# Performance work log

Measured on AMD Instinct MI355X. Metric: run time of the kernel, lower is better.

## Reference

```python
import jax, jax.numpy as jnp
import numpy as np

B = 256      # graph pairs
N = 256      # nodes per graph (uniform -> padding is a reshape)
DEG = 16     # avg degree
D = 32       # one_hot_dim
F1, F2, F3 = 128, 64, 64
T = 16       # tensor_neurons
BINS = 16
BOT = 16     # bottle_neck_neurons


def setup_inputs() -> dict:
    key = jax.random.key(0)
    ks = jax.random.split(key, 24)
    NT = B * N            # total nodes per side
    NE = B * N * DEG      # total directed edges per side
    x_q = jax.random.normal(ks[0], (NT, D), jnp.float32)
    x_c = jax.random.normal(ks[1], (NT, D), jnp.float32)
    edge_q = jax.random.randint(ks[2], (2, NE), 0, NT, jnp.int32)
    edge_c = jax.random.randint(ks[3], (2, NE), 0, NT, jnp.int32)
    qgraph_sizes = jnp.full((B,), N, jnp.int32)
    cgraph_sizes = jnp.full((B,), N, jnp.int32)

    def glorot(k, shape):
        fan = sum(shape[-2:]) if len(shape) >= 2 else shape[0] * 2
        return jax.random.uniform(k, shape, jnp.float32, -1.0, 1.0) * np.sqrt(6.0 / fan)

    params = dict(
        W1=glorot(ks[4], (D, F1)), b1=jnp.zeros((F1,), jnp.float32),
        W2=glorot(ks[5], (F1, F2)), b2=jnp.zeros((F2,), jnp.float32),
        W3=glorot(ks[6], (F2, F3)), b3=jnp.zeros((F3,), jnp.float32),
        attn_w=glorot(ks[7], (F3, F3)),
        ntn_a_w=glorot(ks[8], (T, F3, F3)),
        ntn_b_w=glorot(ks[9], (2 * F3, T)),
        ntn_bias=glorot(ks[10], (T, 1)),
        fc1_w=glorot(ks[11], (T + BINS, BOT)), fc1_b=jnp.zeros((BOT,), jnp.float32),
        fc2_w=glorot(ks[12], (BOT, 1)), fc2_b=jnp.zeros((1,), jnp.float32),
    )
    return dict(x_q=x_q, edge_q=edge_q, x_c=x_c, edge_c=edge_c,
                qgraph_sizes=qgraph_sizes, cgraph_sizes=cgraph_sizes, **params)


def _gcn(x, src, dst, W, b):
    n = x.shape[0]
    h = x @ W
    loop = jnp.arange(n, dtype=src.dtype)
    s = jnp.concatenate([src, loop])
    d = jnp.concatenate([dst, loop])
    deg = jax.ops.segment_sum(jnp.ones(s.shape, h.dtype), d, num_segments=n)
    dinv = jnp.where(deg > 0, jax.lax.rsqrt(jnp.maximum(deg, 1.0)), 0.0)
    coef = (dinv[s] * dinv[d])[:, None]
    return jax.ops.segment_sum(h[s] * coef, d, num_segments=n) + b


def _gnn(x, ei, W1, b1, W2, b2, W3, b3):
    src, dst = ei[0], ei[1]
    h = jax.nn.relu(_gcn(x, src, dst, W1, b1))        # dropout is identity in eval
    h = jax.nn.relu(_gcn(h, src, dst, W2, b2))
    return _gcn(h, src, dst, W3, b3)                  # [B*N, F3]


def _att_pool(q, attn_w, sizes):
    # q: [B, N, F3]
    ctx = jnp.tanh((q.sum(axis=1) @ attn_w) / sizes.astype(q.dtype)[:, None])  # [B, F3]
    sig = jax.nn.sigmoid(jnp.einsum('bnf,bf->bn', q, ctx))                      # [B, N]
    return jnp.einsum('bnf,bn->bf', q, sig)                                     # [B, F3]


def _pair_hist(q, c):
    # per-pair histogram of q @ c^T with BINS bins over each pair's [min, max]
    s = jax.lax.stop_gradient(jnp.einsum('bnf,bmf->bnm', q, c))  # [B, N, N]
    mn = s.min(axis=(1, 2), keepdims=True)
    mx = s.max(axis=(1, 2), keepdims=True)
    idx = jnp.clip(jnp.floor((s - mn) / jnp.maximum(mx - mn, 1e-12) * BINS),
                   0, BINS - 1).astype(jnp.int32)
    gid = (idx + jnp.arange(B, dtype=jnp.int32)[:, None, None] * BINS).reshape(-1)
    h = jax.ops.segment_sum(jnp.ones(gid.shape, jnp.float32), gid,
                            num_segments=B * BINS).reshape(B, BINS)
    return h / h.sum(axis=1, keepdims=True)


def reference(x_q, edge_q, x_c, edge_c, qgraph_sizes, cgraph_sizes,
              W1, b1, W2, b2, W3, b3, attn_w, ntn_a_w, ntn_b_w, ntn_bias,
              fc1_w, fc1_b, fc2_w, fc2_b):
    q = _gnn(x_q, edge_q, W1, b1, W2, b2, W3, b3).reshape(B, N, F3)
    c = _gnn(x_c, edge_c, W1, b1, W2, b2, W3, b3).reshape(B, N, F3)
    e1 = _att_pool(q, attn_w, qgraph_sizes)
    e2 = _att_pool(c, attn_w, cgraph_sizes)
    ntn = (jnp.einsum('bi,tij,bj->bt', e1, ntn_a_w, e2)
           + jnp.concatenate([e1, e2], axis=-1) @ ntn_b_w
           + ntn_bias[:, 0])
    scores = jax.nn.relu(ntn)                                   # [B, T]
    hist = _pair_hist(q, c)                                     # [B, BINS]
    scores = jnp.concatenate([scores, hist], axis=1)
    scores = jax.nn.relu(scores @ fc1_w + fc1_b)
    p = jax.nn.sigmoid(scores @ fc2_w + fc2_b)[:, 0]            # [B]
    ged = -0.5 * (qgraph_sizes + cgraph_sizes).astype(p.dtype) * jnp.log(p)
    return ged
```

## Files before the change

### kernel.cpp

```cpp
#include <hip/hip_runtime.h>
#include <hip/hip_bf16.h>
#include <math.h>

#define BB 256
#define NN 256
#define NT (BB*NN)
#define NT2 (2*NT)
#define NE (NT*16)
#define DD 32
#define F1C 128
#define F2C 64
#define F3C 64
#define TT 16
#define BINS 16

#define NBUCK 256
#define BSHIFT 9
#define BNODES 512
#define BCAP 10240
#define EPB 4096

typedef __attribute__((ext_vector_type(8))) short short8;
typedef __attribute__((ext_vector_type(4))) float f32x4;
typedef __attribute__((ext_vector_type(2))) float f32x2;

__device__ inline float b2f(ushort u) { return __uint_as_float(((uint)u) << 16); }
__device__ inline ushort f2b(float f) {
    uint u = __float_as_uint(f);
    return (ushort)((u + 0x7fffu + ((u >> 16) & 1u)) >> 16);
}
__device__ inline float clamp8(float v) { return fminf(fmaxf(v, -448.0f), 448.0f); }
__device__ inline uchar f2f8(float v) {
    int r = __builtin_amdgcn_cvt_pk_fp8_f32(clamp8(v), 0.0f, 0, false);
    return (uchar)(r & 0xff);
}
__device__ inline void f8x8_acc(uint2 w, float* acc) {
    f32x2 p;
    p = __builtin_amdgcn_cvt_pk_f32_fp8(w.x, false); acc[0] += p.x; acc[1] += p.y;
    p = __builtin_amdgcn_cvt_pk_f32_fp8(w.x, true);  acc[2] += p.x; acc[3] += p.y;
    p = __builtin_amdgcn_cvt_pk_f32_fp8(w.y, false); acc[4] += p.x; acc[5] += p.y;
    p = __builtin_amdgcn_cvt_pk_f32_fp8(w.y, true);  acc[6] += p.x; acc[7] += p.y;
}
__device__ inline uint2 f8x8_pack(const float* v) {
    uint2 r;
    r.x = (uint)__builtin_amdgcn_cvt_pk_fp8_f32(clamp8(v[0]), clamp8(v[1]), 0, false);
    r.x = (uint)__builtin_amdgcn_cvt_pk_fp8_f32(clamp8(v[2]), clamp8(v[3]), (int)r.x, true);
    r.y = (uint)__builtin_amdgcn_cvt_pk_fp8_f32(clamp8(v[4]), clamp8(v[5]), 0, false);
    r.y = (uint)__builtin_amdgcn_cvt_pk_fp8_f32(clamp8(v[6]), clamp8(v[7]), (int)r.y, true);
    return r;
}

__global__ __launch_bounds__(256) void zero_k(int* __restrict__ gcount) {
    gcount[threadIdx.x] = 0;
}

__global__ __launch_bounds__(256) void p1cvt_k(const int* __restrict__ eq, const int* __restrict__ ec,
                                               uint* __restrict__ staged, int* __restrict__ gcount,
                                               const float* __restrict__ a, const float* __restrict__ b,
                                               ushort* __restrict__ out,
                                               const float* __restrict__ W1, const float* __restrict__ W2,
                                               const float* __restrict__ W3, ushort* __restrict__ Wt1,
                                               ushort* __restrict__ Wt2, uchar* __restrict__ Wt3f8) {
    int t = threadIdx.x;
    if (blockIdx.x < 512) {
        __shared__ uint s_pk[EPB];
        __shared__ int s_cnt[NBUCK];
        __shared__ int s_off[NBUCK];
        __shared__ int s_base[NBUCK];
        __shared__ int s_gb[NBUCK];
        bool sideB = blockIdx.x >= 256;
        const int* edge = sideB ? ec : eq;
        int off = sideB ? NT : 0;
        int e0 = (blockIdx.x & 255) * EPB;
        s_cnt[t] = 0;
        __syncthreads();
        uint pk[16]; int bk[16];
#pragma unroll
        for (int j = 0; j < 16; j++) {
            int e = e0 + j * 256 + t;
            int s = edge[e] + off;
            int d = edge[NE + e] + off;
            bk[j] = d >> BSHIFT;
            pk[j] = ((uint)s << BSHIFT) | (uint)(d & (BNODES - 1));
            atomicAdd(&s_cnt[bk[j]], 1);
        }
        __syncthreads();
        s_off[t] = s_cnt[t];
        __syncthreads();
        for (int o = 1; o < NBUCK; o <<= 1) {
            int x = (t >= o) ? s_off[t - o] : 0;
            __syncthreads();
            s_off[t] += x;
            __syncthreads();
        }
        {
            int ex = s_off[t] - s_cnt[t];
            s_base[t] = ex;
            s_off[t] = ex;
            s_gb[t] = atomicAdd(&gcount[t], s_cnt[t]);
        }
        __syncthreads();
#pragma unroll
        for (int j = 0; j < 16; j++) {
            int pos = atomicAdd(&s_off[bk[j]], 1);
            s_pk[pos] = pk[j];
        }
        __syncthreads();
        int w = t >> 6, l = t & 63;
        int bsel = l >> 4, l16 = l & 15;
        for (int pb = w; pb < NBUCK / 4; pb += 4) {
            int bkt = pb * 4 + bsel;
            int n = s_cnt[bkt], st = s_base[bkt], gb = s_gb[bkt];
            if (gb + n > BCAP) n = max(0, BCAP - gb);
            for (int i = l16; i < n; i += 16)
                staged[bkt * BCAP + gb + i] = s_pk[st + i];
        }
    } else if (blockIdx.x < 512 + NT2 * DD / 4 / 256) {
        int i = (blockIdx.x - 512) * 256 + t;
        const int per = NT * DD / 4;
        bool sideB = i >= per;
        const float4* src = (const float4*)(sideB ? b : a);
        float4 v = src[sideB ? i - per : i];
        ushort4 o;
        o.x = f2b(v.x); o.y = f2b(v.y); o.z = f2b(v.z); o.w = f2b(v.w);
        ((ushort4*)out)[i] = o;
    } else {
        int i = (blockIdx.x - (512 + NT2 * DD / 4 / 256)) * 256 + t;
        if (i < DD * F1C)  { int k = i / F1C, n = i % F1C; Wt1[n * DD + k]  = f2b(W1[i]); }
        if (i < F1C * F2C) { int k = i / F2C, n = i % F2C; Wt2[n * F1C + k] = f2b(W2[i]); }
        if (i < F2C * F3C) { int k = i / F3C, n = i % F3C; Wt3f8[n * F2C + k] = f2f8(W3[i]); }
    }
}

__global__ __launch_bounds__(256) void csr_p2_k(const uint* __restrict__ staged, const int* __restrict__ gcount,
                                                int* __restrict__ rp, int* __restrict__ indeg,
                                                float* __restrict__ dinv, int* __restrict__ ep) {
    int b = blockIdx.x;
    int t = threadIdx.x;
    __shared__ int cnt[BNODES];
    __shared__ int fl[BNODES];
    __shared__ int wsum[256];
    __shared__ int gsc[NBUCK];
    cnt[t] = 0; cnt[t + 256] = 0;
    gsc[t] = min(gcount[t], BCAP);
    __syncthreads();
    for (int off = 1; off < NBUCK; off <<= 1) {
        int x = (t >= off) ? gsc[t - off] : 0;
        __syncthreads();
        gsc[t] += x;
        __syncthreads();
    }
    int gbase = (b == 0) ? 0 : gsc[b - 1];
    int n = min(gcount[b], BCAP);
    const uint* sb = staged + (size_t)b * BCAP;
    int i = t;
    for (; i + 768 < n; i += 1024) {
        uint p0 = sb[i];
        uint p1 = sb[i + 256];
        uint p2 = sb[i + 512];
        uint p3 = sb[i + 768];
        atomicAdd(&cnt[p0 & (BNODES - 1)], 1);
        atomicAdd(&cnt[p1 & (BNODES - 1)], 1);
        atomicAdd(&cnt[p2 & (BNODES - 1)], 1);
        atomicAdd(&cnt[p3 & (BNODES - 1)], 1);
    }
    for (; i < n; i += 256)
        atomicAdd(&cnt[sb[i] & (BNODES - 1)], 1);
    __syncthreads();
    int base2 = t * 2;
    int c0 = cnt[base2], c1 = cnt[base2 + 1];
    int s2 = c0 + c1;
    wsum[t] = s2;
    __syncthreads();
    for (int off = 1; off < 256; off <<= 1) {
        int x = (t >= off) ? wsum[t - off] : 0;
        __syncthreads();
        wsum[t] += x;
        __syncthreads();
    }
    int p = gbase + wsum[t] - s2;
    int v0 = b * BNODES + base2;
    rp[v0] = p;          fl[base2] = p;
    indeg[v0] = c0;      dinv[v0] = rsqrtf((float)(c0 + 1));
    p += c0;
    rp[v0 + 1] = p;      fl[base2 + 1] = p;
    indeg[v0 + 1] = c1;  dinv[v0 + 1] = rsqrtf((float)(c1 + 1));
    __syncthreads();
    i = t;
    for (; i + 768 < n; i += 1024) {
        uint p0 = sb[i];
        uint p1 = sb[i + 256];
        uint p2 = sb[i + 512];
        uint p3 = sb[i + 768];
        ep[atomicAdd(&fl[p0 & (BNODES - 1)], 1)] = (int)(p0 >> BSHIFT);
        ep[atomicAdd(&fl[p1 & (BNODES - 1)], 1)] = (int)(p1 >> BSHIFT);
        ep[atomicAdd(&fl[p2 & (BNODES - 1)], 1)] = (int)(p2 >> BSHIFT);
        ep[atomicAdd(&fl[p3 & (BNODES - 1)], 1)] = (int)(p3 >> BSHIFT);
    }
    for (; i < n; i += 256) {
        uint pk = sb[i];
        ep[atomicAdd(&fl[pk & (BNODES - 1)], 1)] = (int)(pk >> BSHIFT);
    }
}

__global__ __launch_bounds__(256) void l1_k(const ushort* __restrict__ xb,
                                            const ushort* __restrict__ Wt1,
                                            const float* __restrict__ b1,
                                            const ushort* __restrict__ Wt2,
                                            const int* __restrict__ rp,
                                            const int* __restrict__ indeg,
                                            const int* __restrict__ ep,
                                            const float* __restrict__ dinv,
                                            uchar* __restrict__ h8a) {
    __shared__ ushort s_x[128][40];
    __shared__ ushort s_h1[128][136];
    int t = threadIdx.x;
    size_t rows0 = (size_t)blockIdx.x * 128;

    int gl = t >> 2;
    int l4 = t & 3;
#pragma unroll
    for (int vt = 0; vt < 2; vt++) {
        int vloc = vt * 64 + gl;
        int v = (int)rows0 + vloc;
        float dv = dinv[v];
        short8 rs = *(const short8*)(xb + (size_t)v * 32 + l4 * 8);
        float acc[8];
#pragma unroll
        for (int j = 0; j < 8; j++) acc[j] = dv * b2f((ushort)rs[j]);
        int start = rp[v];
        int cnt   = indeg[v];
        int i = 0;
        for (; i + 8 <= cnt; i += 8) {
            int sx[8];
#pragma unroll
            for (int j = 0; j < 8; j++) sx[j] = ep[start + i + j];
            float ds[8];
#pragma unroll
            for (int j = 0; j < 8; j++) ds[j] = dinv[sx[j]];
            short8 r[8];
#pragma unroll
            for (int j = 0; j < 8; j++) r[j] = *(const short8*)(xb + (size_t)sx[j] * 32 + l4 * 8);
#pragma unroll
            for (int j = 0; j < 8; j++)
#pragma unroll
                for (int k = 0; k < 8; k++) acc[k] += ds[j] * b2f((ushort)r[j][k]);
        }
        for (; i < cnt; i++) {
            int s0 = ep[start + i];
            float d0 = dinv[s0];
            short8 r0 = *(const short8*)(xb + (size_t)s0 * 32 + l4 * 8);
#pragma unroll
            for (int j = 0; j < 8; j++) acc[j] += d0 * b2f((ushort)r0[j]);
        }
        short8 o;
#pragma unroll
        for (int j = 0; j < 8; j++) o[j] = (short)f2b(dv * acc[j]);
        *(short8*)&s_x[vloc][l4 * 8] = o;
    }
    __syncthreads();

    int w = t >> 6, lane = t & 63;
    int r16 = lane & 15, quad = lane >> 4, koff = quad * 8;

    short8 af1[2];
#pragma unroll
    for (int mt = 0; mt < 2; mt++)
        af1[mt] = *(const short8*)&s_x[(w * 2 + mt) * 16 + r16][koff];
#pragma unroll
    for (int nt = 0; nt < 8; nt++) {
        short8 bfr = *(const short8*)(Wt1 + (size_t)(nt * 16 + r16) * 32 + koff);
        f32x4 acc[2] = {{0.f,0.f,0.f,0.f},{0.f,0.f,0.f,0.f}};
        acc[0] = __builtin_amdgcn_mfma_f32_16x16x32_bf16(af1[0], bfr, acc[0], 0, 0, 0);
        acc[1] = __builtin_amdgcn_mfma_f32_16x16x32_bf16(af1[1], bfr, acc[1], 0, 0, 0);
        int col = nt * 16 + r16;
        float bc = b1[col];
#pragma unroll
        for (int mt = 0; mt < 2; mt++)
#pragma unroll
            for (int r = 0; r < 4; r++) {
                int rl = (w * 2 + mt) * 16 + quad * 4 + r;
                s_h1[rl][col] = f2b(fmaxf(acc[mt][r] + bc, 0.0f));
            }
    }
    __syncthreads();

    short8 af2[4][2];
#pragma unroll
    for (int kc = 0; kc < 4; kc++)
#pragma unroll
        for (int mt = 0; mt < 2; mt++)
            af2[kc][mt] = *(const short8*)&s_h1[(w * 2 + mt) * 16 + r16][kc * 32 + koff];
    float dvr[2][4];
#pragma unroll
    for (int mt = 0; mt < 2; mt++)
#pragma unroll
        for (int r = 0; r < 4; r++)
            dvr[mt][r] = dinv[rows0 + (w * 2 + mt) * 16 + quad * 4 + r];
#pragma unroll
    for (int nt = 0; nt < 4; nt++) {
        f32x4 acc[2] = {{0.f,0.f,0.f,0.f},{0.f,0.f,0.f,0.f}};
#pragma unroll
        for (int kc = 0; kc < 4; kc++) {
            short8 bfr = *(const short8*)(Wt2 + (size_t)(nt * 16 + r16) * 128 + kc * 32 + koff);
            acc[0] = __builtin_amdgcn_mfma_f32_16x16x32_bf16(af2[kc][0], bfr, acc[0], 0, 0, 0);
            acc[1] = __builtin_amdgcn_mfma_f32_16x16x32_bf16(af2[kc][1], bfr, acc[1], 0, 0, 0);
        }
#pragma unroll
        for (int mt = 0; mt < 2; mt++)
#pragma unroll
            for (int r = 0; r < 4; r++) {
                size_t row = rows0 + (w * 2 + mt) * 16 + quad * 4 + r;
                int col = nt * 16 + r16;
                h8a[row * 64 + col] = f2f8(acc[mt][r] * dvr[mt][r]);
            }
    }
}

__global__ __launch_bounds__(256) void l2_k(const uchar* __restrict__ in,
                                            const int* __restrict__ rp,
                                            const int* __restrict__ indeg,
                                            const int* __restrict__ ep,
                                            const float* __restrict__ dinv,
                                            const float* __restrict__ b2,
                                            const uchar* __restrict__ Wt8,
                                            uchar* __restrict__ out8) {
    __shared__ uchar s_a[128][72];
    int t = threadIdx.x;
    size_t rows0 = (size_t)blockIdx.x * 128;

    int g8 = t >> 3;
    int l8 = t & 7;
#pragma unroll
    for (int pass = 0; pass < 4; pass++) {
        int vloc = pass * 32 + g8;
        int v = (int)rows0 + vloc;
        float dv = dinv[v];
        float acc[8] = {0, 0, 0, 0, 0, 0, 0, 0};
        f8x8_acc(*(const uint2*)(in + (size_t)v * 64 + l8 * 8), acc);
        int start = rp[v];
        int cnt   = indeg[v];
        int i = 0;
        for (; i + 8 <= cnt; i += 8) {
            int sx[8];
#pragma unroll
            for (int j = 0; j < 8; j++) sx[j] = ep[start + i + j];
            uint2 gx[8];
#pragma unroll
            for (int j = 0; j < 8; j++) gx[j] = *(const uint2*)(in + (size_t)sx[j] * 64 + l8 * 8);
#pragma unroll
            for (int j = 0; j < 8; j++) f8x8_acc(gx[j], acc);
        }
        for (; i < cnt; i++) {
            int s0 = ep[start + i];
            f8x8_acc(*(const uint2*)(in + (size_t)s0 * 64 + l8 * 8), acc);
        }
#pragma unroll
        for (int j = 0; j < 8; j++)
            acc[j] = fmaxf(dv * acc[j] + b2[l8 * 8 + j], 0.0f);
        *(uint2*)&s_a[vloc][l8 * 8] = f8x8_pack(acc);
    }
    __syncthreads();

    int w = t >> 6, lane = t & 63;
    int r16 = lane & 15, koff = (lane >> 4) * 8;

    long af[2][2];
#pragma unroll
    for (int kc = 0; kc < 2; kc++)
#pragma unroll
        for (int mt = 0; mt < 2; mt++)
            af[kc][mt] = *(const long*)&s_a[(w * 2 + mt) * 16 + r16][kc * 32 + koff];

    float dvr[2][4];
#pragma unroll
    for (int mt = 0; mt < 2; mt++)
#pragma unroll
        for (int r = 0; r < 4; r++)
            dvr[mt][r] = dinv[rows0 + (w * 2 + mt) * 16 + (lane >> 4) * 4 + r];

#pragma unroll
    for (int nt = 0; nt < 4; nt++) {
        f32x4 acc[2] = {{0.f,0.f,0.f,0.f},{0.f,0.f,0.f,0.f}};
#pragma unroll
        for (int kc = 0; kc < 2; kc++) {
            long b = *(const long*)(Wt8 + (size_t)(nt * 16 + r16) * 64 + kc * 32 + koff);
            acc[0] = __builtin_amdgcn_mfma_f32_16x16x32_fp8_fp8(af[kc][0], b, acc[0], 0, 0, 0);
            acc[1] = __builtin_amdgcn_mfma_f32_16x16x32_fp8_fp8(af[kc][1], b, acc[1], 0, 0, 0);
        }
#pragma unroll
        for (int mt = 0; mt < 2; mt++) {
#pragma unroll
            for (int r = 0; r < 4; r++) {
                size_t row = rows0 + (w * 2 + mt) * 16 + (lane >> 4) * 4 + r;
                int col = nt * 16 + (lane & 15);
                out8[row * 64 + col] = f2f8(acc[mt][r] * dvr[mt][r]);
            }
        }
    }
}

template<bool OUT_BF16, bool BIAS, bool RELU>
__global__ __launch_bounds__(256) void agg_f8_k(const uchar* __restrict__ in, const int* __restrict__ rp,
                                                const int* __restrict__ indeg, const int* __restrict__ ep,
                                                const float* __restrict__ dinv,
                                                const float* __restrict__ bias, void* __restrict__ outp) {
    int g = threadIdx.x >> 3;
    int l = threadIdx.x & 7;
    int v = blockIdx.x * 32 + g;
    float dv = dinv[v];
    float acc[8] = {0, 0, 0, 0, 0, 0, 0, 0};
    f8x8_acc(*(const uint2*)(in + (size_t)v * 64 + l * 8), acc);
    int start = rp[v];
    int cnt   = indeg[v];
    int i = 0;
    for (; i + 8 <= cnt; i += 8) {
        int sx[8];
#pragma unroll
        for (int j = 0; j < 8; j++) sx[j] = ep[start + i + j];
        uint2 gx[8];
#pragma unroll
        for (int j = 0; j < 8; j++) gx[j] = *(const uint2*)(in + (size_t)sx[j] * 64 + l * 8);
#pragma unroll
        for (int j = 0; j < 8; j++) f8x8_acc(gx[j], acc);
    }
    for (; i + 4 <= cnt; i += 4) {
        int s0 = ep[start + i];
        int s1 = ep[start + i + 1];
        int s2 = ep[start + i + 2];
        int s3 = ep[start + i + 3];
        uint2 g0 = *(const uint2*)(in + (size_t)s0 * 64 + l * 8);
        uint2 g1 = *(const uint2*)(in + (size_t)s1 * 64 + l * 8);
        uint2 g2 = *(const uint2*)(in + (size_t)s2 * 64 + l * 8);
        uint2 g3 = *(const uint2*)(in + (size_t)s3 * 64 + l * 8);
        f8x8_acc(g0, acc); f8x8_acc(g1, acc); f8x8_acc(g2, acc); f8x8_acc(g3, acc);
    }
    for (; i < cnt; i++) {
        int s0 = ep[start + i];
        f8x8_acc(*(const uint2*)(in + (size_t)s0 * 64 + l * 8), acc);
    }
#pragma unroll
    for (int j = 0; j < 8; j++) {
        float x = dv * acc[j];
        if (BIAS) x += bias[l * 8 + j];
        if (RELU) x = fmaxf(x, 0.0f);
        acc[j] = x;
    }
    if (OUT_BF16) {
        short8 o;
#pragma unroll
        for (int j = 0; j < 8; j++) o[j] = (short)f2b(acc[j]);
        *(short8*)((ushort*)outp + (size_t)v * 64 + l * 8) = o;
    } else {
        *(uint2*)((uchar*)outp + (size_t)v * 64 + l * 8) = f8x8_pack(acc);
    }
}

__global__ __launch_bounds__(256) void pool_hist_k(const ushort* __restrict__ fin,
                                                   const int* __restrict__ qsz, const int* __restrict__ csz,
                                                   const float* __restrict__ attn_w,
                                                   float* __restrict__ e_out, float* __restrict__ histp) {
    __shared__ float smemf[17472];
    int t = threadIdx.x;
    if (blockIdx.x < 512) {
        int b = blockIdx.x & 255;
        bool is_c = blockIdx.x >= BB;
        const ushort* emb = fin + (size_t)blockIdx.x * NN * F3C;
        float size = (float)((is_c ? csz : qsz)[b]);
        float* eo = e_out + (is_c ? BB * F3C : 0) + b * F3C;
        float (*s_emb)[F3C + 1] = (float(*)[F3C + 1])smemf;
        float* s_red = smemf + 256 * 65;
        float* s_sq  = s_red + 256;
        float* s_ctx = s_sq + 64;
        float* s_sig = s_ctx + 64;
        int f = t & 63;
        int w = t >> 6;
#pragma unroll
        for (int it = 0; it < 8; it++) {
            int idx = it * 2048 + t * 8;
            int row = idx >> 6, f0 = idx & 63;
            short8 v = *(const short8*)(emb + idx);
#pragma unroll
            for (int j = 0; j < 8; j++) s_emb[row][f0 + j] = b2f((ushort)v[j]);
        }
        __syncthreads();
        float psum = 0.0f;
#pragma unroll 8
        for (int i2 = 0; i2 < 64; i2++) psum += s_emb[w * 64 + i2][f];
        s_red[w * 64 + f] = psum;
        __syncthreads();
        if (w == 0) {
            s_sq[f] = s_red[f] + s_red[64 + f] + s_red[128 + f] + s_red[192 + f];
            float acc = 0.0f;
            for (int k = 0; k < 64; k++) acc += s_sq[k] * attn_w[k * 64 + f];
            s_ctx[f] = tanhf(acc / size);
        }
        __syncthreads();
        {
            float acc = 0.0f;
#pragma unroll 8
            for (int k = 0; k < 64; k++) acc += s_emb[t][k] * s_ctx[k];
            s_sig[t] = 1.0f / (1.0f + expf(-acc));
        }
        __syncthreads();
        float eacc = 0.0f;
#pragma unroll 8
        for (int i = 0; i < 64; i++) {
            int n = w * 64 + i;
            eacc += s_sig[n] * s_emb[n][f];
        }
        s_red[w * 64 + f] = eacc;
        __syncthreads();
        if (w == 0) eo[f] = s_red[f] + s_red[64 + f] + s_red[128 + f] + s_red[192 + f];
    } else {
        int b = blockIdx.x - 512;
        const ushort* qb = fin + (size_t)b * NN * 64;
        const ushort* cb = fin + (size_t)(NT + b * NN) * 64;
        int lane = t & 63;
        int w = t >> 6;
        int r16 = lane & 15, koff = (lane >> 4) * 8;
        ushort (*cb_s)[72] = (ushort(*)[72])smemf;
        int* h = (int*)(smemf + 9216);
        int* hp = h + 16 * 256;
        float* smn = (float*)(hp + 256);
        float* smx = smn + 4;
        float* s_sc = smx + 4;

#pragma unroll
        for (int it = 0; it < 8; it++) {
            int idx = it * 2048 + t * 8;
            int row = idx >> 6, f0 = idx & 63;
            *(short8*)&cb_s[row][f0] = *(const short8*)(cb + idx);
        }
        short8 a[4][2];
#pragma unroll
        for (int i = 0; i < 4; i++) {
            int row = (w * 4 + i) * 16 + r16;
#pragma unroll
            for (int kk = 0; kk < 2; kk++)
                a[i][kk] = *(const short8*)(qb + row * 64 + kk * 32 + koff);
        }
        __syncthreads();
        float mn = 1e30f, mx = -1e30f;
        for (int mt = 0; mt < 16; mt++) {
            int crow = mt * 16 + r16;
            short8 b0 = *(const short8*)&cb_s[crow][koff];
            short8 b1 = *(const short8*)&cb_s[crow][32 + koff];
#pragma unroll
            for (int i = 0; i < 4; i++) {
                f32x4 acc = {0.0f, 0.0f, 0.0f, 0.0f};
                acc = __builtin_amdgcn_mfma_f32_16x16x32_bf16(a[i][0], b0, acc, 0, 0, 0);
                acc = __builtin_amdgcn_mfma_f32_16x16x32_bf16(a[i][1], b1, acc, 0, 0, 0);
                mn = fminf(mn, fminf(fminf(acc[0], acc[1]), fminf(acc[2], acc[3])));
                mx = fmaxf(mx, fmaxf(fmaxf(acc[0], acc[1]), fmaxf(acc[2], acc[3])));
            }
        }
        for (int off = 32; off; off >>= 1) {
            mn = fminf(mn, __shfl_xor(mn, off, 64));
            mx = fmaxf(mx, __shfl_xor(mx, off, 64));
        }
        if (lane == 0) { smn[w] = mn; smx[w] = mx; }
        __syncthreads();
        if (t == 0) {
            float m0 = fminf(fminf(smn[0], smn[1]), fminf(smn[2], smn[3]));
            float m1 = fmaxf(fmaxf(smx[0], smx[1]), fmaxf(smx[2], smx[3]));
            s_sc[0] = m0;
            s_sc[1] = 16.0f / fmaxf(m1 - m0, 1e-12f);
        }
#pragma unroll
        for (int i = 0; i < 16; i++) h[i * 256 + t] = 0;
        __syncthreads();
        float bmn = s_sc[0], bscale = s_sc[1];
        for (int mt = 0; mt < 16; mt++) {
            int crow = mt * 16 + r16;
            short8 b0 = *(const short8*)&cb_s[crow][koff];
            short8 b1 = *(const short8*)&cb_s[crow][32 + koff];
#pragma unroll
            for (int i = 0; i < 4; i++) {
                f32x4 acc = {0.0f, 0.0f, 0.0f, 0.0f};
                acc = __builtin_amdgcn_mfma_f32_16x16x32_bf16(a[i][0], b0, acc, 0, 0, 0);
                acc = __builtin_amdgcn_mfma_f32_16x16x32_bf16(a[i][1], b1, acc, 0, 0, 0);
#pragma unroll
                for (int r = 0; r < 4; r++) {
                    int bin = (int)floorf((acc[r] - bmn) * bscale);
                    bin = min(max(bin, 0), 15);
                    h[bin * 256 + t] += 1;
                }
            }
        }
        __syncthreads();
        int bb = t >> 4, part = t & 15;
        int sum = 0;
#pragma unroll
        for (int j = 0; j < 16; j++) sum += h[bb * 256 + part * 16 + j];
        hp[bb * 16 + part] = sum;
        __syncthreads();
        if (t < 16) {
            int s = 0;
#pragma unroll
            for (int j = 0; j < 16; j++) s += hp[t * 16 + j];
            histp[b * 16 + t] = (float)s;
        }
    }
}

__global__ __launch_bounds__(256) void ntn_final_k(const float* __restrict__ e, const float* __restrict__ A,
                                                   const float* __restrict__ bw, const float* __restrict__ bias,
                                                   const float* __restrict__ histp,
                                                   const float* __restrict__ fc1w, const float* __restrict__ fc1b,
                                                   const float* __restrict__ fc2w, const float* __restrict__ fc2b,
                                                   const int* __restrict__ qsz, const int* __restrict__ csz,
                                                   float* __restrict__ out) {
    int b = blockIdx.x;
    int t = threadIdx.x;
    int lane = t & 63, w = t >> 6;
    __shared__ float s_e1[64], s_e2[64];
    __shared__ float s_ntn[16];
    __shared__ float s_s[32];
    __shared__ float s_a[16];
    if (t < 64) s_e1[t] = e[b * 64 + t];
    else if (t < 128) s_e2[t - 64] = e[BB * 64 + b * 64 + (t - 64)];
    __syncthreads();
#pragma unroll
    for (int r = 0; r < 4; r++) {
        int idx = t + r * 256;
        const float4* Ar = (const float4*)(A + (size_t)idx * 64);
        float acc = 0.0f;
#pragma unroll
        for (int j = 0; j < 16; j++) {
            float4 a4 = Ar[j];
            acc += a4.x * s_e2[4 * j] + a4.y * s_e2[4 * j + 1]
                 + a4.z * s_e2[4 * j + 2] + a4.w * s_e2[4 * j + 3];
        }
        float p = s_e1[lane] * acc;
        for (int off = 32; off; off >>= 1) p += __shfl_xor(p, off, 64);
        if (lane == 0) s_ntn[w + 4 * r] = p;
    }
    __syncthreads();
    if (t < 16) {
        float acc = s_ntn[t] + bias[t];
        for (int k = 0; k < 64; k++) acc += s_e1[k] * bw[k * 16 + t];
        for (int k = 0; k < 64; k++) acc += s_e2[k] * bw[(64 + k) * 16 + t];
        s_s[t] = fmaxf(acc, 0.0f);
        s_s[16 + t] = histp[b * 16 + t] * (1.0f / 65536.0f);
    }
    __syncthreads();
    if (t < 16) {
        float a = fc1b[t];
        for (int k = 0; k < 32; k++) a += s_s[k] * fc1w[k * 16 + t];
        s_a[t] = fmaxf(a, 0.0f);
    }
    __syncthreads();
    if (t == 0) {
        float z = fc2b[0];
        for (int j = 0; j < 16; j++) z += s_a[j] * fc2w[j];
        float nz = -z;
        float sp = (nz > 20.0f) ? nz : log1pf(expf(nz));
        out[b] = 0.5f * (float)(qsz[b] + csz[b]) * sp;
    }
}

extern "C" void kernel_launch(void* const* d_in, const int* in_sizes, int n_in,
                              void* d_out, int out_size, void* d_ws, size_t ws_size,
                              hipStream_t stream) {
    const float* x_q    = (const float*)d_in[0];
    const int*   edge_q = (const int*)d_in[1];
    const float* x_c    = (const float*)d_in[2];
    const int*   edge_c = (const int*)d_in[3];
    const int*   qsz    = (const int*)d_in[4];
    const int*   csz    = (const int*)d_in[5];
    const float* W1 = (const float*)d_in[6];
    const float* b1 = (const float*)d_in[7];
    const float* W2 = (const float*)d_in[8];
    const float* b2 = (const float*)d_in[9];
    const float* W3 = (const float*)d_in[10];
    const float* b3 = (const float*)d_in[11];
    const float* attn_w  = (const float*)d_in[12];
    const float* ntn_a   = (const float*)d_in[13];
    const float* ntn_b   = (const float*)d_in[14];
    const float* ntn_bias= (const float*)d_in[15];
    const float* fc1w = (const float*)d_in[16];
    const float* fc1b = (const float*)d_in[17];
    const float* fc2w = (const float*)d_in[18];
    const float* fc2b = (const float*)d_in[19];
    float* out = (float*)d_out;

    char* w = (char*)d_ws;
    auto alloc = [&](size_t bytes) -> void* {
        void* p = (void*)w;
        w += (bytes + 255) & ~(size_t)255;
        return p;
    };
    int*    rp     = (int*)alloc((size_t)NT2 * 4);
    int*    indeg  = (int*)alloc((size_t)NT2 * 4);
    float*  dinv   = (float*)alloc((size_t)NT2 * 4);
    int*    gcount = (int*)alloc(NBUCK * 4);
    uint*   staged = (uint*)alloc((size_t)NBUCK * BCAP * 4);
    int*    ep     = (int*)alloc((size_t)2 * NE * 4);
    ushort* xb     = (ushort*)alloc((size_t)NT2 * 32 * 2);
    uchar*  h8a    = (uchar*)alloc((size_t)NT2 * 64);
    uchar*  h8b    = (uchar*)alloc((size_t)NT2 * 64);
    ushort* fin    = (ushort*)alloc((size_t)NT2 * 64 * 2);
    ushort* Wt1    = (ushort*)alloc((size_t)DD * F1C * 2);
    ushort* Wt2    = (ushort*)alloc((size_t)F1C * F2C * 2);
    uchar*  Wt3f8  = (uchar*)alloc((size_t)F2C * F3C);
    float*  e12    = (float*)alloc(2 * BB * 64 * 4);
    float*  histp  = (float*)alloc(256 * 16 * 4);

    zero_k<<<1, 256, 0, stream>>>(gcount);
    p1cvt_k<<<512 + NT2 * DD / 4 / 256 + 32, 256, 0, stream>>>(
        edge_q, edge_c, staged, gcount, x_q, x_c, xb, W1, W2, W3, Wt1, Wt2, Wt3f8);
    csr_p2_k<<<NBUCK, 256, 0, stream>>>(staged, gcount, rp, indeg, dinv, ep);

    l1_k<<<NT2 / 128, 256, 0, stream>>>(xb, Wt1, b1, Wt2, rp, indeg, ep, dinv, h8a);
    l2_k<<<NT2 / 128, 256, 0, stream>>>(h8a, rp, indeg, ep, dinv, b2, Wt3f8, h8b);
    agg_f8_k<true, true, false><<<NT2 / 32, 256, 0, stream>>>(h8b, rp, indeg, ep, dinv, b3, fin);

    pool_hist_k<<<768, 256, 0, stream>>>(fin, qsz, csz, attn_w, e12, histp);
    ntn_final_k<<<BB, 256, 0, stream>>>(e12, ntn_a, ntn_b, ntn_bias, histp,
                                        fc1w, fc1b, fc2w, fc2b, qsz, csz, out);
}
```

Measured before the change: 297.0 us.

## Fuse dinv-prescaled x conversion into CSR pass and halve GCN layer tiles

The bf16 conversion of node features moves from the edge-bucketing kernel into the CSR build kernel. There each row is pre-multiplied by its D^-1/2 factor, so the layer-1 aggregation no longer gathers dinv for every neighbor. Layers 1 and 2 also switch from 128-row to 64-row blocks (one M-tile per wave), which doubles the grid and lowers shared memory and register use. The risks are fewer MFMA reuses of each weight fragment per block, and a longer serial tail in csr_p2_k, which has only 256 blocks.

```diff
diff --git a/kernel.cpp b/kernel.cpp
--- a/kernel.cpp
+++ b/kernel.cpp
@@ -56,8 +56,6 @@
 
 __global__ __launch_bounds__(256) void p1cvt_k(const int* __restrict__ eq, const int* __restrict__ ec,
                                                uint* __restrict__ staged, int* __restrict__ gcount,
-                                               const float* __restrict__ a, const float* __restrict__ b,
-                                               ushort* __restrict__ out,
                                                const float* __restrict__ W1, const float* __restrict__ W2,
                                                const float* __restrict__ W3, ushort* __restrict__ Wt1,
                                                ushort* __restrict__ Wt2, uchar* __restrict__ Wt3f8) {
@@ -115,17 +113,8 @@
             for (int i = l16; i < n; i += 16)
                 staged[bkt * BCAP + gb + i] = s_pk[st + i];
         }
-    } else if (blockIdx.x < 512 + NT2 * DD / 4 / 256) {
+    } else {
         int i = (blockIdx.x - 512) * 256 + t;
-        const int per = NT * DD / 4;
-        bool sideB = i >= per;
-        const float4* src = (const float4*)(sideB ? b : a);
-        float4 v = src[sideB ? i - per : i];
-        ushort4 o;
-        o.x = f2b(v.x); o.y = f2b(v.y); o.z = f2b(v.z); o.w = f2b(v.w);
-        ((ushort4*)out)[i] = o;
-    } else {
-        int i = (blockIdx.x - (512 + NT2 * DD / 4 / 256)) * 256 + t;
         if (i < DD * F1C)  { int k = i / F1C, n = i % F1C; Wt1[n * DD + k]  = f2b(W1[i]); }
         if (i < F1C * F2C) { int k = i / F2C, n = i % F2C; Wt2[n * F1C + k] = f2b(W2[i]); }
         if (i < F2C * F3C) { int k = i / F3C, n = i % F3C; Wt3f8[n * F2C + k] = f2f8(W3[i]); }
@@ -134,13 +123,16 @@
 
 __global__ __launch_bounds__(256) void csr_p2_k(const uint* __restrict__ staged, const int* __restrict__ gcount,
                                                 int* __restrict__ rp, int* __restrict__ indeg,
-                                                float* __restrict__ dinv, int* __restrict__ ep) {
+                                                float* __restrict__ dinv, int* __restrict__ ep,
+                                                const float* __restrict__ xq, const float* __restrict__ xc,
+                                                ushort* __restrict__ xb) {
     int b = blockIdx.x;
     int t = threadIdx.x;
     __shared__ int cnt[BNODES];
     __shared__ int fl[BNODES];
     __shared__ int wsum[256];
     __shared__ int gsc[NBUCK];
+    __shared__ float sdv[BNODES];
     cnt[t] = 0; cnt[t + 256] = 0;
     gsc[t] = min(gcount[t], BCAP);
     __syncthreads();
@@ -180,11 +172,13 @@
     }
     int p = gbase + wsum[t] - s2;
     int v0 = b * BNODES + base2;
+    float d0 = rsqrtf((float)(c0 + 1));
+    float d1 = rsqrtf((float)(c1 + 1));
     rp[v0] = p;          fl[base2] = p;
-    indeg[v0] = c0;      dinv[v0] = rsqrtf((float)(c0 + 1));
+    indeg[v0] = c0;      dinv[v0] = d0;      sdv[base2] = d0;
     p += c0;
     rp[v0 + 1] = p;      fl[base2 + 1] = p;
-    indeg[v0 + 1] = c1;  dinv[v0 + 1] = rsqrtf((float)(c1 + 1));
+    indeg[v0 + 1] = c1;  dinv[v0 + 1] = d1;  sdv[base2 + 1] = d1;
     __syncthreads();
     i = t;
     for (; i + 768 < n; i += 1024) {
@@ -201,6 +195,20 @@
         uint pk = sb[i];
         ep[atomicAdd(&fl[pk & (BNODES - 1)], 1)] = (int)(pk >> BSHIFT);
     }
+    {
+        const float* xs = (b < 128) ? (xq + (size_t)b * BNODES * DD)
+                                    : (xc + ((size_t)b * BNODES - NT) * DD);
+        ushort* xd = xb + (size_t)b * BNODES * DD;
+        for (int g = t; g < BNODES * DD / 4; g += 256) {
+            int r = g >> 3;
+            float4 v = ((const float4*)xs)[g];
+            float dv = sdv[r];
+            ushort4 o;
+            o.x = f2b(v.x * dv); o.y = f2b(v.y * dv);
+            o.z = f2b(v.z * dv); o.w = f2b(v.w * dv);
+            ((ushort4*)xd)[g] = o;
+        }
+    }
 }
 
 __global__ __launch_bounds__(256) void l1_k(const ushort* __restrict__ xb,
@@ -212,22 +220,20 @@
                                             const int* __restrict__ ep,
                                             const float* __restrict__ dinv,
                                             uchar* __restrict__ h8a) {
-    __shared__ ushort s_x[128][40];
-    __shared__ ushort s_h1[128][136];
+    __shared__ ushort s_x[64][40];
+    __shared__ ushort s_h1[64][136];
     int t = threadIdx.x;
-    size_t rows0 = (size_t)blockIdx.x * 128;
-
-    int gl = t >> 2;
-    int l4 = t & 3;
-#pragma unroll
-    for (int vt = 0; vt < 2; vt++) {
-        int vloc = vt * 64 + gl;
-        int v = (int)rows0 + vloc;
+    size_t rows0 = (size_t)blockIdx.x * 64;
+
+    {
+        int gl = t >> 2;
+        int l4 = t & 3;
+        int v = (int)rows0 + gl;
         float dv = dinv[v];
         short8 rs = *(const short8*)(xb + (size_t)v * 32 + l4 * 8);
         float acc[8];
 #pragma unroll
-        for (int j = 0; j < 8; j++) acc[j] = dv * b2f((ushort)rs[j]);
+        for (int j = 0; j < 8; j++) acc[j] = b2f((ushort)rs[j]);
         int start = rp[v];
         int cnt   = indeg[v];
         int i = 0;
@@ -235,85 +241,68 @@
             int sx[8];
 #pragma unroll
             for (int j = 0; j < 8; j++) sx[j] = ep[start + i + j];
-            float ds[8];
-#pragma unroll
-            for (int j = 0; j < 8; j++) ds[j] = dinv[sx[j]];
             short8 r[8];
 #pragma unroll
             for (int j = 0; j < 8; j++) r[j] = *(const short8*)(xb + (size_t)sx[j] * 32 + l4 * 8);
 #pragma unroll
             for (int j = 0; j < 8; j++)
 #pragma unroll
-                for (int k = 0; k < 8; k++) acc[k] += ds[j] * b2f((ushort)r[j][k]);
+                for (int k = 0; k < 8; k++) acc[k] += b2f((ushort)r[j][k]);
         }
         for (; i < cnt; i++) {
             int s0 = ep[start + i];
-            float d0 = dinv[s0];
             short8 r0 = *(const short8*)(xb + (size_t)s0 * 32 + l4 * 8);
 #pragma unroll
-            for (int j = 0; j < 8; j++) acc[j] += d0 * b2f((ushort)r0[j]);
+            for (int j = 0; j < 8; j++) acc[j] += b2f((ushort)r0[j]);
         }
         short8 o;
 #pragma unroll
         for (int j = 0; j < 8; j++) o[j] = (short)f2b(dv * acc[j]);
-        *(short8*)&s_x[vloc][l4 * 8] = o;
+        *(short8*)&s_x[gl][l4 * 8] = o;
     }
     __syncthreads();
 
     int w = t >> 6, lane = t & 63;
     int r16 = lane & 15, quad = lane >> 4, koff = quad * 8;
 
-    short8 af1[2];
-#pragma unroll
-    for (int mt = 0; mt < 2; mt++)
-        af1[mt] = *(const short8*)&s_x[(w * 2 + mt) * 16 + r16][koff];
+    short8 af1 = *(const short8*)&s_x[w * 16 + r16][koff];
 #pragma unroll
     for (int nt = 0; nt < 8; nt++) {
         short8 bfr = *(const short8*)(Wt1 + (size_t)(nt * 16 + r16) * 32 + koff);
-        f32x4 acc[2] = {{0.f,0.f,0.f,0.f},{0.f,0.f,0.f,0.f}};
-        acc[0] = __builtin_amdgcn_mfma_f32_16x16x32_bf16(af1[0], bfr, acc[0], 0, 0, 0);
-        acc[1] = __builtin_amdgcn_mfma_f32_16x16x32_bf16(af1[1], bfr, acc[1], 0, 0, 0);
+        f32x4 acc = {0.f, 0.f, 0.f, 0.f};
+        acc = __builtin_amdgcn_mfma_f32_16x16x32_bf16(af1, bfr, acc, 0, 0, 0);
         int col = nt * 16 + r16;
         float bc = b1[col];
 #pragma unroll
-        for (int mt = 0; mt < 2; mt++)
-#pragma unroll
-            for (int r = 0; r < 4; r++) {
-                int rl = (w * 2 + mt) * 16 + quad * 4 + r;
-                s_h1[rl][col] = f2b(fmaxf(acc[mt][r] + bc, 0.0f));
-            }
-    }
-    __syncthreads();
-
-    short8 af2[4][2];
+        for (int r = 0; r < 4; r++) {
+            int rl = w * 16 + quad * 4 + r;
+            s_h1[rl][col] = f2b(fmaxf(acc[r] + bc, 0.0f));
+        }
+    }
+    __syncthreads();
+
+    short8 af2[4];
 #pragma unroll
     for (int kc = 0; kc < 4; kc++)
-#pragma unroll
-        for (int mt = 0; mt < 2; mt++)
-            af2[kc][mt] = *(const short8*)&s_h1[(w * 2 + mt) * 16 + r16][kc * 32 + koff];
-    float dvr[2][4];
-#pragma unroll
-    for (int mt = 0; mt < 2; mt++)
-#pragma unroll
-        for (int r = 0; r < 4; r++)
-            dvr[mt][r] = dinv[rows0 + (w * 2 + mt) * 16 + quad * 4 + r];
+        af2[kc] = *(const short8*)&s_h1[w * 16 + r16][kc * 32 + koff];
+    float dvr[4];
+#pragma unroll
+    for (int r = 0; r < 4; r++)
+        dvr[r] = dinv[rows0 + w * 16 + quad * 4 + r];
 #pragma unroll
     for (int nt = 0; nt < 4; nt++) {
-        f32x4 acc[2] = {{0.f,0.f,0.f,0.f},{0.f,0.f,0.f,0.f}};
+        f32x4 acc = {0.f, 0.f, 0.f, 0.f};
 #pragma unroll
         for (int kc = 0; kc < 4; kc++) {
             short8 bfr = *(const short8*)(Wt2 + (size_t)(nt * 16 + r16) * 128 + kc * 32 + koff);
-            acc[0] = __builtin_amdgcn_mfma_f32_16x16x32_bf16(af2[kc][0], bfr, acc[0], 0, 0, 0);
-            acc[1] = __builtin_amdgcn_mfma_f32_16x16x32_bf16(af2[kc][1], bfr, acc[1], 0, 0, 0);
-        }
-#pragma unroll
-        for (int mt = 0; mt < 2; mt++)
-#pragma unroll
-            for (int r = 0; r < 4; r++) {
-                size_t row = rows0 + (w * 2 + mt) * 16 + quad * 4 + r;
-                int col = nt * 16 + r16;
-                h8a[row * 64 + col] = f2f8(acc[mt][r] * dvr[mt][r]);
-            }
+            acc = __builtin_amdgcn_mfma_f32_16x16x32_bf16(af2[kc], bfr, acc, 0, 0, 0);
+        }
+#pragma unroll
+        for (int r = 0; r < 4; r++) {
+            size_t row = rows0 + w * 16 + quad * 4 + r;
+            int col = nt * 16 + r16;
+            h8a[row * 64 + col] = f2f8(acc[r] * dvr[r]);
+        }
     }
 }
 
@@ -325,14 +314,14 @@
                                             const float* __restrict__ b2,
                                             const uchar* __restrict__ Wt8,
                                             uchar* __restrict__ out8) {
-    __shared__ uchar s_a[128][72];
+    __shared__ uchar s_a[64][72];
     int t = threadIdx.x;
-    size_t rows0 = (size_t)blockIdx.x * 128;
+    size_t rows0 = (size_t)blockIdx.x * 64;
 
     int g8 = t >> 3;
     int l8 = t & 7;
 #pragma unroll
-    for (int pass = 0; pass < 4; pass++) {
+    for (int pass = 0; pass < 2; pass++) {
         int vloc = pass * 32 + g8;
         int v = (int)rows0 + vloc;
         float dv = dinv[v];
@@ -365,37 +354,29 @@
     int w = t >> 6, lane = t & 63;
     int r16 = lane & 15, koff = (lane >> 4) * 8;
 
-    long af[2][2];
+    long af[2];
 #pragma unroll
     for (int kc = 0; kc < 2; kc++)
-#pragma unroll
-        for (int mt = 0; mt < 2; mt++)
-            af[kc][mt] = *(const long*)&s_a[(w * 2 + mt) * 16 + r16][kc * 32 + koff];
-
-    float dvr[2][4];
-#pragma unroll
-    for (int mt = 0; mt < 2; mt++)
-#pragma unroll
-        for (int r = 0; r < 4; r++)
-            dvr[mt][r] = dinv[rows0 + (w * 2 + mt) * 16 + (lane >> 4) * 4 + r];
+        af[kc] = *(const long*)&s_a[w * 16 + r16][kc * 32 + koff];
+
+    float dvr[4];
+#pragma unroll
+    for (int r = 0; r < 4; r++)
+        dvr[r] = dinv[rows0 + w * 16 + (lane >> 4) * 4 + r];
 
 #pragma unroll
     for (int nt = 0; nt < 4; nt++) {
-        f32x4 acc[2] = {{0.f,0.f,0.f,0.f},{0.f,0.f,0.f,0.f}};
+        f32x4 acc = {0.f, 0.f, 0.f, 0.f};
 #pragma unroll
         for (int kc = 0; kc < 2; kc++) {
             long b = *(const long*)(Wt8 + (size_t)(nt * 16 + r16) * 64 + kc * 32 + koff);
-            acc[0] = __builtin_amdgcn_mfma_f32_16x16x32_fp8_fp8(af[kc][0], b, acc[0], 0, 0, 0);
-            acc[1] = __builtin_amdgcn_mfma_f32_16x16x32_fp8_fp8(af[kc][1], b, acc[1], 0, 0, 0);
-        }
-#pragma unroll
-        for (int mt = 0; mt < 2; mt++) {
-#pragma unroll
-            for (int r = 0; r < 4; r++) {
-                size_t row = rows0 + (w * 2 + mt) * 16 + (lane >> 4) * 4 + r;
-                int col = nt * 16 + (lane & 15);
-                out8[row * 64 + col] = f2f8(acc[mt][r] * dvr[mt][r]);
-            }
+            acc = __builtin_amdgcn_mfma_f32_16x16x32_fp8_fp8(af[kc], b, acc, 0, 0, 0);
+        }
+#pragma unroll
+        for (int r = 0; r < 4; r++) {
+            size_t row = rows0 + w * 16 + (lane >> 4) * 4 + r;
+            int col = nt * 16 + (lane & 15);
+            out8[row * 64 + col] = f2f8(acc[r] * dvr[r]);
         }
     }
 }
@@ -708,12 +689,13 @@
     float*  histp  = (float*)alloc(256 * 16 * 4);
 
     zero_k<<<1, 256, 0, stream>>>(gcount);
-    p1cvt_k<<<512 + NT2 * DD / 4 / 256 + 32, 256, 0, stream>>>(
-        edge_q, edge_c, staged, gcount, x_q, x_c, xb, W1, W2, W3, Wt1, Wt2, Wt3f8);
-    csr_p2_k<<<NBUCK, 256, 0, stream>>>(staged, gcount, rp, indeg, dinv, ep);
-
-    l1_k<<<NT2 / 128, 256, 0, stream>>>(xb, Wt1, b1, Wt2, rp, indeg, ep, dinv, h8a);
-    l2_k<<<NT2 / 128, 256, 0, stream>>>(h8a, rp, indeg, ep, dinv, b2, Wt3f8, h8b);
+    p1cvt_k<<<512 + 32, 256, 0, stream>>>(edge_q, edge_c, staged, gcount,
+                                          W1, W2, W3, Wt1, Wt2, Wt3f8);
+    csr_p2_k<<<NBUCK, 256, 0, stream>>>(staged, gcount, rp, indeg, dinv, ep,
+                                        x_q, x_c, xb);
+
+    l1_k<<<NT2 / 64, 256, 0, stream>>>(xb, Wt1, b1, Wt2, rp, indeg, ep, dinv, h8a);
+    l2_k<<<NT2 / 64, 256, 0, stream>>>(h8a, rp, indeg, ep, dinv, b2, Wt3f8, h8b);
     agg_f8_k<true, true, false><<<NT2 / 32, 256, 0, stream>>>(h8b, rp, indeg, ep, dinv, b3, fin);
 
     pool_hist_k<<<768, 256, 0, stream>>>(fin, qsz, csz, attn_w, e12, histp);
```

After: 291.4 us. No clear change (-1.9%).
